# Performance work log

Hardware: AMD Instinct MI355X
Metric: run time of the kernel (lower is better)

## Reference

```python
import jax, jax.numpy as jnp
import numpy as np

# Architecture constants (match init_kwargs)
NUM_INPUTS = 3      # 2 spatial + 1 time
NUM_SPATIAL = NUM_INPUTS - 1
NUM_LAYERS = 4      # hidden Linear(H,H) blocks
HIDDEN = 256
N_POINTS = 131072
M_DIFF = 1.0        # scalar conductivity M


def setup_inputs() -> dict:
    key = jax.random.key(0)
    ks = jax.random.split(key, 5)
    X = jax.random.uniform(ks[0], (N_POINTS, NUM_INPUTS), dtype=jnp.float32)
    # Xavier-normal weights, zero biases (matches init_method='xavier')
    W_in = jax.random.normal(ks[1], (NUM_INPUTS, HIDDEN), dtype=jnp.float32) * np.sqrt(2.0 / (NUM_INPUTS + HIDDEN))
    b_in = jnp.zeros((HIDDEN,), dtype=jnp.float32)
    W_h = jax.random.normal(ks[2], (NUM_LAYERS, HIDDEN, HIDDEN), dtype=jnp.float32) * np.sqrt(2.0 / (2 * HIDDEN))
    b_h = jnp.zeros((NUM_LAYERS, HIDDEN), dtype=jnp.float32)
    W_out = jax.random.normal(ks[3], (HIDDEN, 1), dtype=jnp.float32) * np.sqrt(2.0 / (HIDDEN + 1))
    b_out = jnp.zeros((1,), dtype=jnp.float32)
    return {"X_collocation": X, "W_in": W_in, "b_in": b_in,
            "W_h": W_h, "b_h": b_h, "W_out": W_out, "b_out": b_out}


def reference(X_collocation, W_in, b_in, W_h, b_h, W_out, b_out):
    """Faithful translation of MonodomainSolverPINNs.pde with use_ode=False,
    scalar M, no source term: residual = dv/dt - M * Laplacian_spatial(v).
    Returns (pde_loss, ode_loss)."""

    def mlp_scalar(x):  # x: [NUM_INPUTS] -> scalar v
        h = jnp.tanh(x @ W_in + b_in)
        for i in range(NUM_LAYERS):  # static small loop over layers
            h = jnp.tanh(h @ W_h[i] + b_h[i])
        return (h @ W_out + b_out)[0]

    grad_fn = jax.grad(mlp_scalar)

    def derivs(x):
        # forward-over-reverse: one reverse pass for grad, one JVP per spatial dim
        g = grad_fn(x)                       # [NUM_INPUTS]
        diag = []
        for i in range(NUM_SPATIAL):
            e = jnp.zeros((NUM_INPUTS,), dtype=x.dtype).at[i].set(1.0)
            _, hv = jax.jvp(grad_fn, (x,), (e,))
            diag.append(hv[i])               # d^2v/dx_i^2
        return g[-1], jnp.stack(diag).sum()  # dv/dt, spatial laplacian

    dv_dt, laplacian = jax.vmap(derivs)(X_collocation)  # each [N]
    diffusion = M_DIFF * laplacian
    residual = dv_dt - diffusion                        # reaction term = 0
    pde_loss = jnp.mean(residual ** 2)
    ode_loss = jnp.float32(0.0)
    return (pde_loss, ode_loss)
```

## Files before the change

### kernel.cpp

```cpp
#include <hip/hip_runtime.h>
#include <hip/hip_bf16.h>

typedef __attribute__((ext_vector_type(8))) short  short8;
typedef __attribute__((ext_vector_type(4))) float  f32x4;

#define HIDDEN   256
#define NLAYERS  4
#define NPTS     131072
#define PPW      16
#define NWG      (NPTS / PPW)
#define NSTATE   4
#define PLANE    32768

#define WS_PARTIALS   0
#define WS_WHI        65536

__device__ __forceinline__ unsigned short f2bf(float f) {
    return __builtin_bit_cast(unsigned short, __float2bfloat16(f));
}
__device__ __forceinline__ float bf2f(unsigned short h) {
    return __uint_as_float(((unsigned)h) << 16);
}
__device__ __forceinline__ unsigned pack2(float a, float b) {
    __hip_bfloat162 h2 = __float22bfloat162_rn(make_float2(a, b));
    unsigned u;
    __builtin_memcpy(&u, &h2, sizeof(u));
    return u;
}
__device__ __forceinline__ float fast_tanh(float z) {
    float e = __expf(2.f * z);
    return 1.f - __fdividef(2.f, e + 1.f);
}

__global__ void prep_w(const float* __restrict__ Wh, unsigned short* __restrict__ whi)
{
    int b    = blockIdx.x;
    int lay  = b >> 7;
    int jt   = (b >> 3) & 15;
    int kt   = b & 7;
    int lane = threadIdx.x;
    int j    = jt * 16 + (lane & 15);
    int k0   = kt * 32 + (lane >> 4) * 8;
    const float* W = Wh + lay * 65536;
    int base = ((lay * 16 + jt) * 8 + kt) * 512 + lane * 8;
#pragma unroll
    for (int e = 0; e < 8; ++e)
        whi[base + e] = f2bf(W[(k0 + e) * HIDDEN + j]);
}

__global__ __launch_bounds__(1024, 8)
void pinn_mfma(const float* __restrict__ X,
               const float* __restrict__ W_in, const float* __restrict__ b_in,
               const float* __restrict__ b_h,  const float* __restrict__ W_out,
               const unsigned short* __restrict__ whi,
               double* __restrict__ partials)
{
    extern __shared__ char lds[];
    float*  red = (float*)lds;
    double* sq  = (double*)(lds + 4096);

    const int tid  = threadIdx.x;
    const int lane = tid & 63;
    const int swid = __builtin_amdgcn_readfirstlane(tid >> 6);
    const int q    = lane >> 4;
    const int p_   = lane & 15;
    const int wg   = blockIdx.x;
    const int pt0  = wg * PPW;

    {
        const int p  = tid & 15;
        const int jq = tid >> 4;
        const int j0 = jq * 4;
        const float* xp = X + (pt0 + p) * 3;
        const float x0 = xp[0], x1 = xp[1], x2 = xp[2];
        const f32x4 w0 = *(const f32x4*)(W_in + j0);
        const f32x4 w1 = *(const f32x4*)(W_in + HIDDEN + j0);
        const f32x4 w2 = *(const f32x4*)(W_in + 2 * HIDDEN + j0);
        const f32x4 bq = *(const f32x4*)(b_in + j0);
        float o[NSTATE][4];
#pragma unroll
        for (int r = 0; r < 4; ++r) {
            float z  = fmaf(x0, w0[r], fmaf(x1, w1[r], fmaf(x2, w2[r], bq[r])));
            float a  = fast_tanh(z);
            float td = 1.f - a * a;
            float t2 = 2.f * a * td;
            float sw = fmaf(w0[r], w0[r], w1[r] * w1[r]);
            o[0][r] = a;
            o[1][r] = td * w0[r];
            o[2][r] = td * w1[r];
            o[3][r] = fmaf(td, w2[r], t2 * sw);
        }
        const int kt = j0 >> 5, kg = (j0 >> 3) & 3, e0 = j0 & 7;
        const int sub = (kg * 16 + p) * 16 + e0 * 2;
#pragma unroll
        for (int s = 0; s < NSTATE; ++s) {
            uint2 wv = { pack2(o[s][0], o[s][1]), pack2(o[s][2], o[s][3]) };
            *(uint2*)(lds + (s * 8 + kt) * 1024 + sub) = wv;
        }
    }
    __syncthreads();

#pragma unroll 1
    for (int l = 0; l < NLAYERS; ++l) {
        const char* sbase = lds + lane * 16;
        const unsigned short* wbh = whi + (l * 16 + swid) * 4096 + lane * 8;

        const f32x4 bias = *(const f32x4*)(b_h + l * HIDDEN + swid * 16 + q * 4);

        f32x4 acc[NSTATE];
#pragma unroll
        for (int mt = 0; mt < NSTATE; ++mt)
            acc[mt] = (f32x4){0.f, 0.f, 0.f, 0.f};

#pragma unroll 2
        for (int kt = 0; kt < 8; ++kt) {
            short8 wh = *(const short8*)(wbh + kt * 512);
            short8 sh_[NSTATE];
#pragma unroll
            for (int mt = 0; mt < NSTATE; ++mt)
                sh_[mt] = *(const short8*)(sbase + (mt * 8 + kt) * 1024);

            __builtin_amdgcn_s_setprio(1);
#pragma unroll
            for (int mt = 0; mt < NSTATE; ++mt)
                acc[mt] = __builtin_amdgcn_mfma_f32_16x16x32_bf16(wh, sh_[mt], acc[mt], 0, 0, 0);
            __builtin_amdgcn_s_setprio(0);
        }

        __syncthreads();

        {
            const int j0 = swid * 16 + q * 4;
            const int kt = j0 >> 5, kg = (j0 >> 3) & 3, e0 = j0 & 7;
            const int sub = (kg * 16 + p_) * 16 + e0 * 2;
            float o[NSTATE][4];
#pragma unroll
            for (int r = 0; r < 4; ++r) {
                float z0 = acc[0][r] + bias[r];
                float z1 = acc[1][r], z2 = acc[2][r], zc = acc[3][r];
                float a  = fast_tanh(z0);
                float td = 1.f - a * a;
                float t2 = 2.f * a * td;
                o[0][r] = a;
                o[1][r] = td * z1;
                o[2][r] = td * z2;
                o[3][r] = fmaf(td, zc, t2 * fmaf(z1, z1, z2 * z2));
            }
            const int sLo = (l < NLAYERS - 1) ? 0 : 3;
#pragma unroll
            for (int s = 0; s < NSTATE; ++s) {
                if (s < sLo) continue;
                uint2 wv = { pack2(o[s][0], o[s][1]), pack2(o[s][2], o[s][3]) };
                *(uint2*)(lds + (s * 8 + kt) * 1024 + sub) = wv;
            }
        }
        __syncthreads();
    }

    {
        const int p    = tid & 15;
        const int jseg = tid >> 4;
        const int j0   = jseg * 4;
        const int kt = j0 >> 5, kg = (j0 >> 3) & 3, e0 = j0 & 7;
        const int sub = (kg * 16 + p) * 16 + e0 * 2;
        uint2 cv = *(uint2*)(lds + (3 * 8 + kt) * 1024 + sub);
        f32x4 wo = *(const f32x4*)(W_out + j0);
        float sum;
        sum = fmaf(wo[0], bf2f((unsigned short)(cv.x & 0xFFFF)), 0.f);
        sum = fmaf(wo[1], bf2f((unsigned short)(cv.x >> 16)),    sum);
        sum = fmaf(wo[2], bf2f((unsigned short)(cv.y & 0xFFFF)), sum);
        sum = fmaf(wo[3], bf2f((unsigned short)(cv.y >> 16)),    sum);
        __syncthreads();
        red[jseg * 16 + p] = sum;
    }
    __syncthreads();
    if (tid < PPW) {
        float s = 0.f;
        for (int g = 0; g < 64; ++g) s += red[g * 16 + tid];
        double d = (double)s;
        sq[tid] = d * d;
    }
    __syncthreads();
    if (tid == 0) {
        double tot = 0.0;
        for (int p = 0; p < PPW; ++p) tot += sq[p];
        partials[wg] = tot;
    }
}

__global__ void pinn_reduce_kernel(const double* __restrict__ partials, float* __restrict__ out)
{
    __shared__ double sh[256];
    double t = 0.0;
    for (int i = 0; i < NWG / 256; ++i) t += partials[threadIdx.x * (NWG / 256) + i];
    sh[threadIdx.x] = t;
    __syncthreads();
    for (int ofs = 128; ofs > 0; ofs >>= 1) {
        if ((int)threadIdx.x < ofs) sh[threadIdx.x] += sh[threadIdx.x + ofs];
        __syncthreads();
    }
    if (threadIdx.x == 0) {
        out[0] = (float)(sh[0] / (double)NPTS);
        out[1] = 0.f;
    }
}

extern "C" void kernel_launch(void* const* d_in, const int* in_sizes, int n_in,
                              void* d_out, int out_size, void* d_ws, size_t ws_size,
                              hipStream_t stream)
{
    const float* X     = (const float*)d_in[0];
    const float* W_in  = (const float*)d_in[1];
    const float* b_in  = (const float*)d_in[2];
    const float* W_h   = (const float*)d_in[3];
    const float* b_h   = (const float*)d_in[4];
    const float* W_out = (const float*)d_in[5];

    double*         partials = (double*)((char*)d_ws + WS_PARTIALS);
    unsigned short* whi      = (unsigned short*)((char*)d_ws + WS_WHI);
    float*          out      = (float*)d_out;

    const size_t lds_bytes = PLANE;
    (void)hipFuncSetAttribute((const void*)pinn_mfma,
                              hipFuncAttributeMaxDynamicSharedMemorySize, (int)lds_bytes);

    hipLaunchKernelGGL(prep_w, dim3(512), dim3(64), 0, stream, W_h, whi);
    hipLaunchKernelGGL(pinn_mfma, dim3(NWG), dim3(1024), lds_bytes, stream,
                       X, W_in, b_in, b_h, W_out, whi, partials);
    hipLaunchKernelGGL(pinn_reduce_kernel, dim3(1), dim3(256), 0, stream,
                       partials, out);
}
```

Before: 342.3 us.

## Ping-pong two point batches to overlap tanh epilogue with MFMA GEMM

```diff
diff --git a/kernel.cpp b/kernel.cpp
--- a/kernel.cpp
+++ b/kernel.cpp
@@ -6,8 +6,8 @@
 
 #define HIDDEN   256
 #define NLAYERS  4
+#define PPW      32
 #define NPTS     131072
-#define PPW      16
 #define NWG      (NPTS / PPW)
 #define NSTATE   4
 #define PLANE    32768
@@ -48,7 +48,56 @@
         whi[base + e] = f2bf(W[(k0 + e) * HIDDEN + j]);
 }
 
-__global__ __launch_bounds__(1024, 8)
+#define GEMM_QTR(ACC, PBASE, WB, KT0)                                                    \
+    _Pragma("unroll")                                                                    \
+    for (int kt = (KT0); kt < (KT0) + 4; ++kt) {                                         \
+        short8 wh0 = *(const short8*)((WB) + 0 * 4096 + kt * 512);                       \
+        short8 wh1 = *(const short8*)((WB) + 1 * 4096 + kt * 512);                       \
+        short8 s_[NSTATE];                                                               \
+        _Pragma("unroll")                                                                \
+        for (int mt = 0; mt < NSTATE; ++mt)                                              \
+            s_[mt] = *(const short8*)((PBASE) + lane * 16 + (mt * 8 + kt) * 1024);       \
+        __builtin_amdgcn_s_setprio(1);                                                   \
+        _Pragma("unroll")                                                                \
+        for (int mt = 0; mt < NSTATE; ++mt) {                                            \
+            ACC[0][mt] = __builtin_amdgcn_mfma_f32_16x16x32_bf16(wh0, s_[mt], ACC[0][mt], 0, 0, 0); \
+            ACC[1][mt] = __builtin_amdgcn_mfma_f32_16x16x32_bf16(wh1, s_[mt], ACC[1][mt], 0, 0, 0); \
+        }                                                                                \
+        __builtin_amdgcn_s_setprio(0);                                                   \
+    }
+
+#define TANH_UNIT(ACC, POUT, JJ, BIAS, SLO)                                              \
+    {                                                                                    \
+        const int j0 = (swid * 2 + (JJ)) * 16 + q * 4;                                   \
+        const int kt = j0 >> 5, kg = (j0 >> 3) & 3, e0 = j0 & 7;                         \
+        const int sub = (kg * 16 + p_) * 16 + e0 * 2;                                    \
+        float o[NSTATE][4];                                                              \
+        _Pragma("unroll")                                                                \
+        for (int r = 0; r < 4; ++r) {                                                    \
+            float z0 = ACC[JJ][0][r] + (BIAS)[r];                                        \
+            float z1 = ACC[JJ][1][r], z2 = ACC[JJ][2][r], zc = ACC[JJ][3][r];            \
+            float a  = fast_tanh(z0);                                                    \
+            float td = 1.f - a * a;                                                      \
+            float t2 = 2.f * a * td;                                                     \
+            o[0][r] = a; o[1][r] = td * z1; o[2][r] = td * z2;                           \
+            o[3][r] = fmaf(td, zc, t2 * fmaf(z1, z1, z2 * z2));                          \
+        }                                                                                \
+        _Pragma("unroll")                                                                \
+        for (int s = 0; s < NSTATE; ++s) {                                               \
+            if (s < (SLO)) continue;                                                     \
+            uint2 wv = { pack2(o[s][0], o[s][1]), pack2(o[s][2], o[s][3]) };             \
+            *(uint2*)((POUT) + (s * 8 + kt) * 1024 + sub) = wv;                          \
+        }                                                                                \
+    }
+
+#define ACC_ZERO(ACC)                                                                    \
+    _Pragma("unroll")                                                                    \
+    for (int jj = 0; jj < 2; ++jj)                                                       \
+        _Pragma("unroll")                                                                \
+        for (int mt = 0; mt < NSTATE; ++mt)                                              \
+            ACC[jj][mt] = (f32x4){0.f, 0.f, 0.f, 0.f};
+
+__global__ __launch_bounds__(512, 4)
 void pinn_mfma(const float* __restrict__ X,
                const float* __restrict__ W_in, const float* __restrict__ b_in,
                const float* __restrict__ b_h,  const float* __restrict__ W_out,
@@ -56,6 +105,8 @@
                double* __restrict__ partials)
 {
     extern __shared__ char lds[];
+    char*   PA  = lds;
+    char*   PB  = lds + PLANE;
     float*  red = (float*)lds;
     double* sq  = (double*)(lds + 4096);
 
@@ -68,115 +119,115 @@
     const int pt0  = wg * PPW;
 
     {
-        const int p  = tid & 15;
-        const int jq = tid >> 4;
-        const int j0 = jq * 4;
-        const float* xp = X + (pt0 + p) * 3;
-        const float x0 = xp[0], x1 = xp[1], x2 = xp[2];
-        const f32x4 w0 = *(const f32x4*)(W_in + j0);
-        const f32x4 w1 = *(const f32x4*)(W_in + HIDDEN + j0);
-        const f32x4 w2 = *(const f32x4*)(W_in + 2 * HIDDEN + j0);
-        const f32x4 bq = *(const f32x4*)(b_in + j0);
-        float o[NSTATE][4];
-#pragma unroll
-        for (int r = 0; r < 4; ++r) {
-            float z  = fmaf(x0, w0[r], fmaf(x1, w1[r], fmaf(x2, w2[r], bq[r])));
-            float a  = fast_tanh(z);
-            float td = 1.f - a * a;
-            float t2 = 2.f * a * td;
-            float sw = fmaf(w0[r], w0[r], w1[r] * w1[r]);
-            o[0][r] = a;
-            o[1][r] = td * w0[r];
-            o[2][r] = td * w1[r];
-            o[3][r] = fmaf(td, w2[r], t2 * sw);
-        }
-        const int kt = j0 >> 5, kg = (j0 >> 3) & 3, e0 = j0 & 7;
-        const int sub = (kg * 16 + p) * 16 + e0 * 2;
-#pragma unroll
-        for (int s = 0; s < NSTATE; ++s) {
-            uint2 wv = { pack2(o[s][0], o[s][1]), pack2(o[s][2], o[s][3]) };
-            *(uint2*)(lds + (s * 8 + kt) * 1024 + sub) = wv;
-        }
+        const int p   = tid & 15;
+        const int jq0 = tid >> 4;
+#pragma unroll
+        for (int bl = 0; bl < 2; ++bl) {
+            char* P = bl ? PB : PA;
+            const float* xp = X + (pt0 + bl * 16 + p) * 3;
+            const float x0 = xp[0], x1 = xp[1], x2 = xp[2];
+#pragma unroll
+            for (int i = 0; i < 2; ++i) {
+                const int jq = jq0 + 32 * i;
+                const int j0 = jq * 4;
+                const f32x4 w0 = *(const f32x4*)(W_in + j0);
+                const f32x4 w1 = *(const f32x4*)(W_in + HIDDEN + j0);
+                const f32x4 w2 = *(const f32x4*)(W_in + 2 * HIDDEN + j0);
+                const f32x4 bq = *(const f32x4*)(b_in + j0);
+                float o[NSTATE][4];
+#pragma unroll
+                for (int r = 0; r < 4; ++r) {
+                    float z  = fmaf(x0, w0[r], fmaf(x1, w1[r], fmaf(x2, w2[r], bq[r])));
+                    float a  = fast_tanh(z);
+                    float td = 1.f - a * a;
+                    float t2 = 2.f * a * td;
+                    float sw = fmaf(w0[r], w0[r], w1[r] * w1[r]);
+                    o[0][r] = a;
+                    o[1][r] = td * w0[r];
+                    o[2][r] = td * w1[r];
+                    o[3][r] = fmaf(td, w2[r], t2 * sw);
+                }
+                const int kt = j0 >> 5, kg = (j0 >> 3) & 3, e0 = j0 & 7;
+                const int sub = (kg * 16 + p) * 16 + e0 * 2;
+#pragma unroll
+                for (int s = 0; s < NSTATE; ++s) {
+                    uint2 wv = { pack2(o[s][0], o[s][1]), pack2(o[s][2], o[s][3]) };
+                    *(uint2*)(P + (s * 8 + kt) * 1024 + sub) = wv;
+                }
+            }
+        }
+    }
+    __syncthreads();
+
+    f32x4 accA[2][NSTATE], accB[2][NSTATE];
+
+    {
+        const unsigned short* wb = whi + (0 * 16 + swid * 2) * 4096 + lane * 8;
+        ACC_ZERO(accA);
+        GEMM_QTR(accA, PA, wb, 0);
+        GEMM_QTR(accA, PA, wb, 4);
     }
     __syncthreads();
 
 #pragma unroll 1
     for (int l = 0; l < NLAYERS; ++l) {
-        const char* sbase = lds + lane * 16;
-        const unsigned short* wbh = whi + (l * 16 + swid) * 4096 + lane * 8;
-
-        const f32x4 bias = *(const f32x4*)(b_h + l * HIDDEN + swid * 16 + q * 4);
-
-        f32x4 acc[NSTATE];
-#pragma unroll
-        for (int mt = 0; mt < NSTATE; ++mt)
-            acc[mt] = (f32x4){0.f, 0.f, 0.f, 0.f};
-
-#pragma unroll 2
-        for (int kt = 0; kt < 8; ++kt) {
-            short8 wh = *(const short8*)(wbh + kt * 512);
-            short8 sh_[NSTATE];
-#pragma unroll
-            for (int mt = 0; mt < NSTATE; ++mt)
-                sh_[mt] = *(const short8*)(sbase + (mt * 8 + kt) * 1024);
-
-            __builtin_amdgcn_s_setprio(1);
-#pragma unroll
-            for (int mt = 0; mt < NSTATE; ++mt)
-                acc[mt] = __builtin_amdgcn_mfma_f32_16x16x32_bf16(wh, sh_[mt], acc[mt], 0, 0, 0);
-            __builtin_amdgcn_s_setprio(0);
-        }
-
+        const int sLo = (l < NLAYERS - 1) ? 0 : 3;
+        const f32x4 bs0 = *(const f32x4*)(b_h + l * HIDDEN + (swid * 2 + 0) * 16 + q * 4);
+        const f32x4 bs1 = *(const f32x4*)(b_h + l * HIDDEN + (swid * 2 + 1) * 16 + q * 4);
+
+        {
+            const unsigned short* wb = whi + (l * 16 + swid * 2) * 4096 + lane * 8;
+            ACC_ZERO(accB);
+            GEMM_QTR(accB, PB, wb, 0);
+            TANH_UNIT(accA, PA, 0, bs0, sLo);
+            GEMM_QTR(accB, PB, wb, 4);
+            TANH_UNIT(accA, PA, 1, bs1, sLo);
+        }
         __syncthreads();
 
-        {
-            const int j0 = swid * 16 + q * 4;
+        if (l < NLAYERS - 1) {
+            const unsigned short* wb = whi + ((l + 1) * 16 + swid * 2) * 4096 + lane * 8;
+            ACC_ZERO(accA);
+            GEMM_QTR(accA, PA, wb, 0);
+            TANH_UNIT(accB, PB, 0, bs0, sLo);
+            GEMM_QTR(accA, PA, wb, 4);
+            TANH_UNIT(accB, PB, 1, bs1, sLo);
+        } else {
+            TANH_UNIT(accB, PB, 0, bs0, sLo);
+            TANH_UNIT(accB, PB, 1, bs1, sLo);
+        }
+        __syncthreads();
+    }
+
+    {
+        const int p   = tid & 15;
+        const int jq0 = tid >> 4;
+        float sumA = 0.f, sumB = 0.f;
+#pragma unroll
+        for (int i = 0; i < 2; ++i) {
+            const int jq = jq0 + 32 * i, j0 = jq * 4;
             const int kt = j0 >> 5, kg = (j0 >> 3) & 3, e0 = j0 & 7;
-            const int sub = (kg * 16 + p_) * 16 + e0 * 2;
-            float o[NSTATE][4];
-#pragma unroll
-            for (int r = 0; r < 4; ++r) {
-                float z0 = acc[0][r] + bias[r];
-                float z1 = acc[1][r], z2 = acc[2][r], zc = acc[3][r];
-                float a  = fast_tanh(z0);
-                float td = 1.f - a * a;
-                float t2 = 2.f * a * td;
-                o[0][r] = a;
-                o[1][r] = td * z1;
-                o[2][r] = td * z2;
-                o[3][r] = fmaf(td, zc, t2 * fmaf(z1, z1, z2 * z2));
-            }
-            const int sLo = (l < NLAYERS - 1) ? 0 : 3;
-#pragma unroll
-            for (int s = 0; s < NSTATE; ++s) {
-                if (s < sLo) continue;
-                uint2 wv = { pack2(o[s][0], o[s][1]), pack2(o[s][2], o[s][3]) };
-                *(uint2*)(lds + (s * 8 + kt) * 1024 + sub) = wv;
-            }
-        }
-        __syncthreads();
-    }
-
-    {
-        const int p    = tid & 15;
-        const int jseg = tid >> 4;
-        const int j0   = jseg * 4;
-        const int kt = j0 >> 5, kg = (j0 >> 3) & 3, e0 = j0 & 7;
-        const int sub = (kg * 16 + p) * 16 + e0 * 2;
-        uint2 cv = *(uint2*)(lds + (3 * 8 + kt) * 1024 + sub);
-        f32x4 wo = *(const f32x4*)(W_out + j0);
-        float sum;
-        sum = fmaf(wo[0], bf2f((unsigned short)(cv.x & 0xFFFF)), 0.f);
-        sum = fmaf(wo[1], bf2f((unsigned short)(cv.x >> 16)),    sum);
-        sum = fmaf(wo[2], bf2f((unsigned short)(cv.y & 0xFFFF)), sum);
-        sum = fmaf(wo[3], bf2f((unsigned short)(cv.y >> 16)),    sum);
-        __syncthreads();
-        red[jseg * 16 + p] = sum;
+            const int sub = (kg * 16 + p) * 16 + e0 * 2;
+            uint2 cA = *(uint2*)(PA + (3 * 8 + kt) * 1024 + sub);
+            uint2 cB = *(uint2*)(PB + (3 * 8 + kt) * 1024 + sub);
+            f32x4 wo = *(const f32x4*)(W_out + j0);
+            sumA = fmaf(wo[0], bf2f((unsigned short)(cA.x & 0xFFFF)), sumA);
+            sumA = fmaf(wo[1], bf2f((unsigned short)(cA.x >> 16)),    sumA);
+            sumA = fmaf(wo[2], bf2f((unsigned short)(cA.y & 0xFFFF)), sumA);
+            sumA = fmaf(wo[3], bf2f((unsigned short)(cA.y >> 16)),    sumA);
+            sumB = fmaf(wo[0], bf2f((unsigned short)(cB.x & 0xFFFF)), sumB);
+            sumB = fmaf(wo[1], bf2f((unsigned short)(cB.x >> 16)),    sumB);
+            sumB = fmaf(wo[2], bf2f((unsigned short)(cB.y & 0xFFFF)), sumB);
+            sumB = fmaf(wo[3], bf2f((unsigned short)(cB.y >> 16)),    sumB);
+        }
+        red[jq0 * 16 + p]       = sumA;
+        red[512 + jq0 * 16 + p] = sumB;
     }
     __syncthreads();
     if (tid < PPW) {
+        const int base = (tid >> 4) * 512, p = tid & 15;
         float s = 0.f;
-        for (int g = 0; g < 64; ++g) s += red[g * 16 + tid];
+        for (int g = 0; g < 32; ++g) s += red[base + g * 16 + p];
         double d = (double)s;
         sq[tid] = d * d;
     }
@@ -220,12 +271,12 @@
     unsigned short* whi      = (unsigned short*)((char*)d_ws + WS_WHI);
     float*          out      = (float*)d_out;
 
-    const size_t lds_bytes = PLANE;
+    const size_t lds_bytes = 2 * PLANE;
     (void)hipFuncSetAttribute((const void*)pinn_mfma,
                               hipFuncAttributeMaxDynamicSharedMemorySize, (int)lds_bytes);
 
     hipLaunchKernelGGL(prep_w, dim3(512), dim3(64), 0, stream, W_h, whi);
-    hipLaunchKernelGGL(pinn_mfma, dim3(NWG), dim3(1024), lds_bytes, stream,
+    hipLaunchKernelGGL(pinn_mfma, dim3(NWG), dim3(512), lds_bytes, stream,
                        X, W_in, b_in, b_h, W_out, whi, partials);
     hipLaunchKernelGGL(pinn_reduce_kernel, dim3(1), dim3(256), 0, stream,
                        partials, out);
```

After: 355.0 us. 3.7% more time.
